# Performance work log

Hardware: AMD Instinct MI355X
Metric: run time of the kernel (lower is better)

Reference implementation:

```python
import jax, jax.numpy as jnp
import numpy as np

SCALE = 100.0  # sharp-softmax temperature from the torch module

def _build_tables():
    # ByteToNibbleFFN: W1 is identity(256) so it is mathematically a no-op; keep W2.
    W2_b2n = np.zeros((256, 32), np.float32)
    bb = np.arange(256)
    W2_b2n[bb, bb >> 4] = 1.0
    W2_b2n[bb, 16 + (bb & 15)] = 1.0
    # NibbleAddWithCarryFFN tables
    W1_add = np.zeros((34, 512), np.float32)
    W2_sum = np.zeros((512, 16), np.float32)
    W2_cout = np.zeros((512, 2), np.float32)
    for a in range(16):
        for b in range(16):
            for c in range(2):
                idx = a * 32 + b * 2 + c
                W1_add[a, idx] = 1.0
                W1_add[16 + b, idx] = 1.0
                W1_add[32 + c, idx] = 1.0
                t = a + b + c
                W2_sum[idx, t & 15] = 1.0
                W2_cout[idx, 1 if t > 15 else 0] = 1.0
    # NibbleToByteFFN tables
    W1_n2b = np.zeros((32, 256), np.float32)
    W2_n2b = np.zeros((256, 256), np.float32)
    for h in range(16):
        for l in range(16):
            addr = h * 16 + l
            W1_n2b[h, addr] = 1.0
            W1_n2b[16 + l, addr] = 1.0
            W2_n2b[addr, (h << 4) | l] = 1.0
    return tuple(jnp.asarray(t) for t in (W2_b2n, W1_add, W2_sum, W2_cout, W1_n2b, W2_n2b))

W2_B2N, W1_ADD, W2_SUM, W2_COUT, W1_N2B, W2_N2B = _build_tables()

def _b2n(x):
    # byte [.,256] -> (high [.,16], low [.,16]); W1=eye(256) omitted (identity)
    out = x @ W2_B2N
    return out[..., :16], out[..., 16:]

def _nib_add(a, b, cin):
    combined = jnp.concatenate([a, b, cin], axis=-1)           # [.,34]
    address = jax.nn.softmax(combined @ W1_ADD * SCALE, axis=-1)  # [.,512]
    return address @ W2_SUM, address @ W2_COUT

def _n2b(high, low):
    combined = jnp.concatenate([high, low], axis=-1)           # [.,32]
    address = jax.nn.softmax(combined @ W1_N2B * SCALE, axis=-1)  # [.,256]
    return address @ W2_N2B

def setup_inputs() -> dict:
    key = jax.random.key(0)
    k1, k2 = jax.random.split(key)
    B = 32768
    a = jax.random.uniform(k1, (B, 4, 256), dtype=jnp.float32)
    b = jax.random.uniform(k2, (B, 4, 256), dtype=jnp.float32)
    return {"a": a, "b": b}

def reference(a, b):
    # NeuralALU.add: ripple-carry add over 4 bytes, 2 nibble adds per byte
    B = a.shape[0]
    carry = jnp.zeros((B, 2), a.dtype).at[:, 0].set(1.0)  # carry_zero one-hot
    out_bytes = []
    for i in range(4):  # fixed structural loop over bytes (carry dependence)
        ah, al = _b2n(a[:, i])
        bh, bl = _b2n(b[:, i])
        sl, carry = _nib_add(al, bl, carry)
        sh, carry = _nib_add(ah, bh, carry)
        out_bytes.append(_n2b(sh, sl))
    return jnp.stack(out_bytes, axis=1)  # [B,4,256]
```

## Files before the change

### kernel.cpp

```cpp
#include <hip/hip_runtime.h>

#define NIB_SCALE 100.0f

template<int CTRL>
__device__ __forceinline__ float fdpp(float x) {
    return __int_as_float(__builtin_amdgcn_update_dpp(
        0, __float_as_int(x), CTRL, 0xF, 0xF, true));
}

__device__ __forceinline__ float rsum16d(float v) {
    v += fdpp<0x121>(v); v += fdpp<0x122>(v); v += fdpp<0x124>(v); v += fdpp<0x128>(v);
    return v;
}
__device__ __forceinline__ float rmax16d(float v) {
    v = fmaxf(v, fdpp<0x121>(v)); v = fmaxf(v, fdpp<0x122>(v));
    v = fmaxf(v, fdpp<0x124>(v)); v = fmaxf(v, fdpp<0x128>(v));
    return v;
}
__device__ __forceinline__ float scan16d(float v) {
    v += fdpp<0x111>(v); v += fdpp<0x112>(v); v += fdpp<0x114>(v); v += fdpp<0x118>(v);
    return v;
}
__device__ __forceinline__ float softmax16d(float v) {
    float m = rmax16d(v);
    float e = __expf(NIB_SCALE * (v - m));
    float s = rsum16d(e);
    return e / s;
}
__device__ __forceinline__ float sharp_sigmoid(float c) {
    return 1.0f / (1.0f + __expf(NIB_SCALE * (1.0f - 2.0f * c)));
}

#define GATHER_ROT(dst, src)            \
    dst[0]  = (src);                    \
    dst[1]  = fdpp<0x121>(src);         \
    dst[2]  = fdpp<0x122>(src);         \
    dst[3]  = fdpp<0x123>(src);         \
    dst[4]  = fdpp<0x124>(src);         \
    dst[5]  = fdpp<0x125>(src);         \
    dst[6]  = fdpp<0x126>(src);         \
    dst[7]  = fdpp<0x127>(src);         \
    dst[8]  = fdpp<0x128>(src);         \
    dst[9]  = fdpp<0x129>(src);         \
    dst[10] = fdpp<0x12A>(src);         \
    dst[11] = fdpp<0x12B>(src);         \
    dst[12] = fdpp<0x12C>(src);         \
    dst[13] = fdpp<0x12D>(src);         \
    dst[14] = fdpp<0x12E>(src);         \
    dst[15] = fdpp<0x12F>(src);

__global__ __launch_bounds__(256) void nalu_kernel(const float* __restrict__ A,
                                                   const float* __restrict__ B,
                                                   float* __restrict__ O,
                                                   int nrows) {
    __shared__ __align__(16) float sQL[16][16];
    __shared__ __align__(16) float sQH[16][16];
    __shared__ __align__(16) float sPSL[16][16];
    __shared__ __align__(16) float sPSH[16][16];
    __shared__ __align__(16) float sOV[4][4][4];

    const int tid = threadIdx.x;
    const int k = tid & 15;
    const int g = tid >> 4;
    const int b = g & 3;
    const int w = tid >> 6;
    const int row = blockIdx.x * 4 + w;
    if (row >= nrows) return;
    const long base = (long)row * 1024 + b * 256;

    const float* pa = A + base;
    const float* pb = B + base;

    float a0 = 0, a1 = 0, a2 = 0, a3 = 0, b0 = 0, b1 = 0, b2 = 0, b3 = 0;
    #pragma unroll
    for (int e = 0; e < 4; ++e) {
        a0 += pa[16 * e + k];        b0 += pb[16 * e + k];
        a1 += pa[16 * (e + 4) + k];  b1 += pb[16 * (e + 4) + k];
        a2 += pa[16 * (e + 8) + k];  b2 += pb[16 * (e + 8) + k];
        a3 += pa[16 * (e + 12) + k]; b3 += pb[16 * (e + 12) + k];
    }
    float al = (a0 + a1) + (a2 + a3);
    float bl = (b0 + b1) + (b2 + b3);
    const float4* pa4 = (const float4*)(pa + 16 * k);
    const float4* pb4 = (const float4*)(pb + 16 * k);
    float4 ra0 = pa4[0], ra1 = pa4[1], ra2 = pa4[2], ra3 = pa4[3];
    float4 rb0 = pb4[0], rb1 = pb4[1], rb2 = pb4[2], rb3 = pb4[3];
    float ah = ((ra0.x + ra0.y) + (ra0.z + ra0.w)) + ((ra1.x + ra1.y) + (ra1.z + ra1.w))
             + ((ra2.x + ra2.y) + (ra2.z + ra2.w)) + ((ra3.x + ra3.y) + (ra3.z + ra3.w));
    float bh = ((rb0.x + rb0.y) + (rb0.z + rb0.w)) + ((rb1.x + rb1.y) + (rb1.z + rb1.w))
             + ((rb2.x + rb2.y) + (rb2.z + rb2.w)) + ((rb3.x + rb3.y) + (rb3.z + rb3.w));

    float pal = softmax16d(al);
    float pbl = softmax16d(bl);
    float pah = softmax16d(ah);
    float pbh = softmax16d(bh);

    sQL[g][k] = pbl;
    sQH[g][k] = pbh;

    float mirl = fdpp<0x140>(pbl);
    float mirh = fdpp<0x140>(pbh);
    float T15l = scan16d(mirl);
    float T15h = scan16d(mirh);
    float ov15l = rsum16d(pal * T15l);
    float c15l  = rsum16d(pal * mirl);
    float ov15h = rsum16d(pah * T15h);
    float c15h  = rsum16d(pah * mirh);
    float ov16l = ov15l - c15l;
    float ov16h = ov15h - c15h;

    sOV[w][0][b] = ov16l;
    sOV[w][1][b] = ov15l;
    sOV[w][2][b] = ov16h;
    sOV[w][3][b] = ov15h;

    float QL[16], QH[16];
    *(float4*)&QL[0]  = *(const float4*)&sQL[g][0];
    *(float4*)&QL[4]  = *(const float4*)&sQL[g][4];
    *(float4*)&QL[8]  = *(const float4*)&sQL[g][8];
    *(float4*)&QL[12] = *(const float4*)&sQL[g][12];
    float GL[16];
    GATHER_ROT(GL, pal)
    float rl = 0.f;
    #pragma unroll
    for (int j = 0; j < 16; ++j) rl = fmaf(GL[j], QL[j], rl);

    *(float4*)&QH[0]  = *(const float4*)&sQH[g][0];
    *(float4*)&QH[4]  = *(const float4*)&sQH[g][4];
    *(float4*)&QH[8]  = *(const float4*)&sQH[g][8];
    *(float4*)&QH[12] = *(const float4*)&sQH[g][12];
    float GH[16];
    GATHER_ROT(GH, pah)
    float rh = 0.f;
    #pragma unroll
    for (int j = 0; j < 16; ++j) rh = fmaf(GH[j], QH[j], rh);

    float4 O16L = *(const float4*)&sOV[w][0][0];
    float4 O15L = *(const float4*)&sOV[w][1][0];
    float4 O16H = *(const float4*)&sOV[w][2][0];
    float4 O15H = *(const float4*)&sOV[w][3][0];

    float qc1_0 = sharp_sigmoid(O16L.x);
    float qc0_0 = 1.f - qc1_0;
    float pc1_1 = sharp_sigmoid(qc0_0 * O16H.x + qc1_0 * O15H.x);
    float pc0_1 = 1.f - pc1_1;
    float qc1_1 = sharp_sigmoid(pc0_1 * O16L.y + pc1_1 * O15L.y);
    float qc0_1 = 1.f - qc1_1;
    float pc1_2 = sharp_sigmoid(qc0_1 * O16H.y + qc1_1 * O15H.y);
    float pc0_2 = 1.f - pc1_2;
    float qc1_2 = sharp_sigmoid(pc0_2 * O16L.z + pc1_2 * O15L.z);
    float qc0_2 = 1.f - qc1_2;
    float pc1_3 = sharp_sigmoid(qc0_2 * O16H.z + qc1_2 * O15H.z);
    float pc0_3 = 1.f - pc1_3;
    float qc1_3 = sharp_sigmoid(pc0_3 * O16L.w + pc1_3 * O15L.w);
    float qc0_3 = 1.f - qc1_3;

    float pc0 = b == 0 ? 1.f   : b == 1 ? pc0_1 : b == 2 ? pc0_2 : pc0_3;
    float pc1 = b == 0 ? 0.f   : b == 1 ? pc1_1 : b == 2 ? pc1_2 : pc1_3;
    float qc0 = b == 0 ? qc0_0 : b == 1 ? qc0_1 : b == 2 ? qc0_2 : qc0_3;
    float qc1 = b == 0 ? qc1_0 : b == 1 ? qc1_1 : b == 2 ? qc1_2 : qc1_3;

    float slow  = pc0 * rl + pc1 * fdpp<0x121>(rl);
    float shigh = qc0 * rh + qc1 * fdpp<0x121>(rh);

    float psl = softmax16d(slow);
    float psh = softmax16d(shigh);
    sPSL[g][k] = psl;
    sPSH[g][k] = psh;

    float4 pslq = *(const float4*)&sPSL[g][4 * (k & 3)];
    float* po = O + base;
    #pragma unroll
    for (int c = 0; c < 4; ++c) {
        float hs = sPSH[g][4 * c + (k >> 2)];
        float4 o4 = make_float4(hs * pslq.x, hs * pslq.y, hs * pslq.z, hs * pslq.w);
        *(float4*)(po + 64 * c + 4 * k) = o4;
    }
}

extern "C" void kernel_launch(void* const* d_in, const int* in_sizes, int n_in,
                              void* d_out, int out_size, void* d_ws, size_t ws_size,
                              hipStream_t stream) {
    const float* A = (const float*)d_in[0];
    const float* B = (const float*)d_in[1];
    float* O = (float*)d_out;
    int nrows = in_sizes[0] / 1024;
    int grid = (nrows + 3) / 4;
    nalu_kernel<<<grid, 256, 0, stream>>>(A, B, O, nrows);
}
```

Before: 306.8 us.

## Use persistent grid-stride waves with register prefetch of next row and nontemporal stores

Caps the grid at 1024 blocks and turns each wave into a persistent worker that loops over rows with a grid stride. Global loads for the next row are issued into registers before the current row is computed, to overlap memory latency with the softmax and carry work. Output stores become nontemporal. The register double-buffering raises register pressure, which launch_bounds(256,4) tries to keep in check, and fewer resident waves may reduce latency hiding on a bandwidth-bound kernel.

```diff
diff --git a/kernel.cpp b/kernel.cpp
--- a/kernel.cpp
+++ b/kernel.cpp
@@ -1,6 +1,8 @@
 #include <hip/hip_runtime.h>
 
 #define NIB_SCALE 100.0f
+
+typedef float vfloat4 __attribute__((ext_vector_type(4)));
 
 template<int CTRL>
 __device__ __forceinline__ float fdpp(float x) {
@@ -49,10 +51,10 @@
     dst[14] = fdpp<0x12E>(src);         \
     dst[15] = fdpp<0x12F>(src);
 
-__global__ __launch_bounds__(256) void nalu_kernel(const float* __restrict__ A,
-                                                   const float* __restrict__ B,
-                                                   float* __restrict__ O,
-                                                   int nrows) {
+__global__ __launch_bounds__(256, 4) void nalu_kernel(const float* __restrict__ A,
+                                                      const float* __restrict__ B,
+                                                      float* __restrict__ O,
+                                                      int nrows) {
     __shared__ __align__(16) float sQL[16][16];
     __shared__ __align__(16) float sQH[16][16];
     __shared__ __align__(16) float sPSL[16][16];
@@ -64,117 +66,137 @@
     const int g = tid >> 4;
     const int b = g & 3;
     const int w = tid >> 6;
-    const int row = blockIdx.x * 4 + w;
-    if (row >= nrows) return;
-    const long base = (long)row * 1024 + b * 256;
-
-    const float* pa = A + base;
-    const float* pb = B + base;
-
-    float a0 = 0, a1 = 0, a2 = 0, a3 = 0, b0 = 0, b1 = 0, b2 = 0, b3 = 0;
-    #pragma unroll
-    for (int e = 0; e < 4; ++e) {
-        a0 += pa[16 * e + k];        b0 += pb[16 * e + k];
-        a1 += pa[16 * (e + 4) + k];  b1 += pb[16 * (e + 4) + k];
-        a2 += pa[16 * (e + 8) + k];  b2 += pb[16 * (e + 8) + k];
-        a3 += pa[16 * (e + 12) + k]; b3 += pb[16 * (e + 12) + k];
-    }
-    float al = (a0 + a1) + (a2 + a3);
-    float bl = (b0 + b1) + (b2 + b3);
-    const float4* pa4 = (const float4*)(pa + 16 * k);
-    const float4* pb4 = (const float4*)(pb + 16 * k);
-    float4 ra0 = pa4[0], ra1 = pa4[1], ra2 = pa4[2], ra3 = pa4[3];
-    float4 rb0 = pb4[0], rb1 = pb4[1], rb2 = pb4[2], rb3 = pb4[3];
-    float ah = ((ra0.x + ra0.y) + (ra0.z + ra0.w)) + ((ra1.x + ra1.y) + (ra1.z + ra1.w))
-             + ((ra2.x + ra2.y) + (ra2.z + ra2.w)) + ((ra3.x + ra3.y) + (ra3.z + ra3.w));
-    float bh = ((rb0.x + rb0.y) + (rb0.z + rb0.w)) + ((rb1.x + rb1.y) + (rb1.z + rb1.w))
-             + ((rb2.x + rb2.y) + (rb2.z + rb2.w)) + ((rb3.x + rb3.y) + (rb3.z + rb3.w));
-
-    float pal = softmax16d(al);
-    float pbl = softmax16d(bl);
-    float pah = softmax16d(ah);
-    float pbh = softmax16d(bh);
-
-    sQL[g][k] = pbl;
-    sQH[g][k] = pbh;
-
-    float mirl = fdpp<0x140>(pbl);
-    float mirh = fdpp<0x140>(pbh);
-    float T15l = scan16d(mirl);
-    float T15h = scan16d(mirh);
-    float ov15l = rsum16d(pal * T15l);
-    float c15l  = rsum16d(pal * mirl);
-    float ov15h = rsum16d(pah * T15h);
-    float c15h  = rsum16d(pah * mirh);
-    float ov16l = ov15l - c15l;
-    float ov16h = ov15h - c15h;
-
-    sOV[w][0][b] = ov16l;
-    sOV[w][1][b] = ov15l;
-    sOV[w][2][b] = ov16h;
-    sOV[w][3][b] = ov15h;
-
-    float QL[16], QH[16];
-    *(float4*)&QL[0]  = *(const float4*)&sQL[g][0];
-    *(float4*)&QL[4]  = *(const float4*)&sQL[g][4];
-    *(float4*)&QL[8]  = *(const float4*)&sQL[g][8];
-    *(float4*)&QL[12] = *(const float4*)&sQL[g][12];
-    float GL[16];
-    GATHER_ROT(GL, pal)
-    float rl = 0.f;
-    #pragma unroll
-    for (int j = 0; j < 16; ++j) rl = fmaf(GL[j], QL[j], rl);
-
-    *(float4*)&QH[0]  = *(const float4*)&sQH[g][0];
-    *(float4*)&QH[4]  = *(const float4*)&sQH[g][4];
-    *(float4*)&QH[8]  = *(const float4*)&sQH[g][8];
-    *(float4*)&QH[12] = *(const float4*)&sQH[g][12];
-    float GH[16];
-    GATHER_ROT(GH, pah)
-    float rh = 0.f;
-    #pragma unroll
-    for (int j = 0; j < 16; ++j) rh = fmaf(GH[j], QH[j], rh);
-
-    float4 O16L = *(const float4*)&sOV[w][0][0];
-    float4 O15L = *(const float4*)&sOV[w][1][0];
-    float4 O16H = *(const float4*)&sOV[w][2][0];
-    float4 O15H = *(const float4*)&sOV[w][3][0];
-
-    float qc1_0 = sharp_sigmoid(O16L.x);
-    float qc0_0 = 1.f - qc1_0;
-    float pc1_1 = sharp_sigmoid(qc0_0 * O16H.x + qc1_0 * O15H.x);
-    float pc0_1 = 1.f - pc1_1;
-    float qc1_1 = sharp_sigmoid(pc0_1 * O16L.y + pc1_1 * O15L.y);
-    float qc0_1 = 1.f - qc1_1;
-    float pc1_2 = sharp_sigmoid(qc0_1 * O16H.y + qc1_1 * O15H.y);
-    float pc0_2 = 1.f - pc1_2;
-    float qc1_2 = sharp_sigmoid(pc0_2 * O16L.z + pc1_2 * O15L.z);
-    float qc0_2 = 1.f - qc1_2;
-    float pc1_3 = sharp_sigmoid(qc0_2 * O16H.z + qc1_2 * O15H.z);
-    float pc0_3 = 1.f - pc1_3;
-    float qc1_3 = sharp_sigmoid(pc0_3 * O16L.w + pc1_3 * O15L.w);
-    float qc0_3 = 1.f - qc1_3;
-
-    float pc0 = b == 0 ? 1.f   : b == 1 ? pc0_1 : b == 2 ? pc0_2 : pc0_3;
-    float pc1 = b == 0 ? 0.f   : b == 1 ? pc1_1 : b == 2 ? pc1_2 : pc1_3;
-    float qc0 = b == 0 ? qc0_0 : b == 1 ? qc0_1 : b == 2 ? qc0_2 : qc0_3;
-    float qc1 = b == 0 ? qc1_0 : b == 1 ? qc1_1 : b == 2 ? qc1_2 : qc1_3;
-
-    float slow  = pc0 * rl + pc1 * fdpp<0x121>(rl);
-    float shigh = qc0 * rh + qc1 * fdpp<0x121>(rh);
-
-    float psl = softmax16d(slow);
-    float psh = softmax16d(shigh);
-    sPSL[g][k] = psl;
-    sPSH[g][k] = psh;
-
-    float4 pslq = *(const float4*)&sPSL[g][4 * (k & 3)];
-    float* po = O + base;
-    #pragma unroll
-    for (int c = 0; c < 4; ++c) {
-        float hs = sPSH[g][4 * c + (k >> 2)];
-        float4 o4 = make_float4(hs * pslq.x, hs * pslq.y, hs * pslq.z, hs * pslq.w);
-        *(float4*)(po + 64 * c + 4 * k) = o4;
+    const int wave0 = blockIdx.x * 4 + w;
+    const int wstride = gridDim.x * 4;
+    if (wave0 >= nrows) return;
+
+    float cA[16], cB[16];
+    float4 rA[4], rB[4];
+
+    long cur = (long)wave0 * 1024 + b * 256;
+    const long bstr = (long)wstride * 1024;
+
+    auto issue = [&](long bb) {
+        const float* pa = A + bb;
+        const float* pb = B + bb;
+        #pragma unroll
+        for (int h = 0; h < 16; ++h) { cA[h] = pa[16 * h + k]; cB[h] = pb[16 * h + k]; }
+        const float4* pa4 = (const float4*)(pa + 16 * k);
+        const float4* pb4 = (const float4*)(pb + 16 * k);
+        #pragma unroll
+        for (int j = 0; j < 4; ++j) { rA[j] = pa4[j]; rB[j] = pb4[j]; }
+    };
+
+    issue(cur);
+
+    for (int row = wave0; row < nrows; row += wstride) {
+        float a0 = 0, a1 = 0, a2 = 0, a3 = 0, b0 = 0, b1 = 0, b2 = 0, b3 = 0;
+        #pragma unroll
+        for (int e = 0; e < 4; ++e) {
+            a0 += cA[e];        b0 += cB[e];
+            a1 += cA[e + 4];    b1 += cB[e + 4];
+            a2 += cA[e + 8];    b2 += cB[e + 8];
+            a3 += cA[e + 12];   b3 += cB[e + 12];
+        }
+        float al = (a0 + a1) + (a2 + a3);
+        float bl = (b0 + b1) + (b2 + b3);
+        float ah = ((rA[0].x + rA[0].y) + (rA[0].z + rA[0].w)) + ((rA[1].x + rA[1].y) + (rA[1].z + rA[1].w))
+                 + ((rA[2].x + rA[2].y) + (rA[2].z + rA[2].w)) + ((rA[3].x + rA[3].y) + (rA[3].z + rA[3].w));
+        float bh = ((rB[0].x + rB[0].y) + (rB[0].z + rB[0].w)) + ((rB[1].x + rB[1].y) + (rB[1].z + rB[1].w))
+                 + ((rB[2].x + rB[2].y) + (rB[2].z + rB[2].w)) + ((rB[3].x + rB[3].y) + (rB[3].z + rB[3].w));
+
+        const long mybase = cur;
+        const long nxt = (row + wstride < nrows) ? cur + bstr : cur;
+        issue(nxt);
+        cur = nxt;
+
+        float pal = softmax16d(al);
+        float pbl = softmax16d(bl);
+        float pah = softmax16d(ah);
+        float pbh = softmax16d(bh);
+
+        sQL[g][k] = pbl;
+        sQH[g][k] = pbh;
+
+        float mirl = fdpp<0x140>(pbl);
+        float mirh = fdpp<0x140>(pbh);
+        float T15l = scan16d(mirl);
+        float T15h = scan16d(mirh);
+        float ov15l = rsum16d(pal * T15l);
+        float c15l  = rsum16d(pal * mirl);
+        float ov15h = rsum16d(pah * T15h);
+        float c15h  = rsum16d(pah * mirh);
+        float ov16l = ov15l - c15l;
+        float ov16h = ov15h - c15h;
+
+        sOV[w][0][b] = ov16l;
+        sOV[w][1][b] = ov15l;
+        sOV[w][2][b] = ov16h;
+        sOV[w][3][b] = ov15h;
+
+        float QL[16], QH[16];
+        *(float4*)&QL[0]  = *(const float4*)&sQL[g][0];
+        *(float4*)&QL[4]  = *(const float4*)&sQL[g][4];
+        *(float4*)&QL[8]  = *(const float4*)&sQL[g][8];
+        *(float4*)&QL[12] = *(const float4*)&sQL[g][12];
+        float GL[16];
+        GATHER_ROT(GL, pal)
+        float rl = 0.f;
+        #pragma unroll
+        for (int j = 0; j < 16; ++j) rl = fmaf(GL[j], QL[j], rl);
+
+        *(float4*)&QH[0]  = *(const float4*)&sQH[g][0];
+        *(float4*)&QH[4]  = *(const float4*)&sQH[g][4];
+        *(float4*)&QH[8]  = *(const float4*)&sQH[g][8];
+        *(float4*)&QH[12] = *(const float4*)&sQH[g][12];
+        float GH[16];
+        GATHER_ROT(GH, pah)
+        float rh = 0.f;
+        #pragma unroll
+        for (int j = 0; j < 16; ++j) rh = fmaf(GH[j], QH[j], rh);
+
+        float4 O16L = *(const float4*)&sOV[w][0][0];
+        float4 O15L = *(const float4*)&sOV[w][1][0];
+        float4 O16H = *(const float4*)&sOV[w][2][0];
+        float4 O15H = *(const float4*)&sOV[w][3][0];
+
+        float qc1_0 = sharp_sigmoid(O16L.x);
+        float qc0_0 = 1.f - qc1_0;
+        float pc1_1 = sharp_sigmoid(qc0_0 * O16H.x + qc1_0 * O15H.x);
+        float pc0_1 = 1.f - pc1_1;
+        float qc1_1 = sharp_sigmoid(pc0_1 * O16L.y + pc1_1 * O15L.y);
+        float qc0_1 = 1.f - qc1_1;
+        float pc1_2 = sharp_sigmoid(qc0_1 * O16H.y + qc1_1 * O15H.y);
+        float pc0_2 = 1.f - pc1_2;
+        float qc1_2 = sharp_sigmoid(pc0_2 * O16L.z + pc1_2 * O15L.z);
+        float qc0_2 = 1.f - qc1_2;
+        float pc1_3 = sharp_sigmoid(qc0_2 * O16H.z + qc1_2 * O15H.z);
+        float pc0_3 = 1.f - pc1_3;
+        float qc1_3 = sharp_sigmoid(pc0_3 * O16L.w + pc1_3 * O15L.w);
+        float qc0_3 = 1.f - qc1_3;
+
+        float pc0 = b == 0 ? 1.f   : b == 1 ? pc0_1 : b == 2 ? pc0_2 : pc0_3;
+        float pc1 = b == 0 ? 0.f   : b == 1 ? pc1_1 : b == 2 ? pc1_2 : pc1_3;
+        float qc0 = b == 0 ? qc0_0 : b == 1 ? qc0_1 : b == 2 ? qc0_2 : qc0_3;
+        float qc1 = b == 0 ? qc1_0 : b == 1 ? qc1_1 : b == 2 ? qc1_2 : qc1_3;
+
+        float slow  = pc0 * rl + pc1 * fdpp<0x121>(rl);
+        float shigh = qc0 * rh + qc1 * fdpp<0x121>(rh);
+
+        float psl = softmax16d(slow);
+        float psh = softmax16d(shigh);
+        sPSL[g][k] = psl;
+        sPSH[g][k] = psh;
+
+        float4 pslq = *(const float4*)&sPSL[g][4 * (k & 3)];
+        float* po = O + mybase;
+        #pragma unroll
+        for (int c = 0; c < 4; ++c) {
+            float hs = sPSH[g][4 * c + (k >> 2)];
+            vfloat4 o4;
+            o4.x = hs * pslq.x; o4.y = hs * pslq.y; o4.z = hs * pslq.z; o4.w = hs * pslq.w;
+            __builtin_nontemporal_store(o4, (vfloat4*)(po + 64 * c + 4 * k));
+        }
     }
 }
 
@@ -186,5 +208,6 @@
     float* O = (float*)d_out;
     int nrows = in_sizes[0] / 1024;
     int grid = (nrows + 3) / 4;
+    if (grid > 1024) grid = 1024;
     nalu_kernel<<<grid, 256, 0, stream>>>(A, B, O, nrows);
 }
```

Result: slower. 323.3 us (+5.4%).
